# Kernel tuning notes

Hardware: AMD Instinct MI355X
Metric: run time of the kernel (lower is better)

## Reference

```python
import jax, jax.numpy as jnp
import numpy as np

N_BINS = 15
NUM_CLASSES = 16


def _risk_from_H2(u):
    # torch: 0.5*(1 - sqrt(clamp(2*2^-u - 1, min=0)))
    inner = 2.0 * jnp.exp2(-u) - 1.0
    pos = inner > 0.0
    s = jnp.sqrt(jnp.where(pos, inner, 1.0))  # safe sqrt (grad 0 where clamped)
    return 0.5 * (1.0 - jnp.where(pos, s, 0.0))


def setup_inputs() -> dict:
    key = jax.random.key(0)
    k1, k2 = jax.random.split(key)
    N = 4194304
    logits = jax.random.normal(k1, (N, NUM_CLASSES), dtype=jnp.float32)
    labels = jax.random.randint(k2, (N,), 0, NUM_CLASSES)
    return {"logits": logits, "labels": labels}


def reference(logits, labels):
    # logits: [N, C]; labels: [N]
    probs = jax.nn.softmax(logits, axis=-1)                     # [N, C]
    H2 = -jnp.log2((probs * probs).sum(-1) + 1e-12)             # [N]
    err_real = (jnp.argmax(probs, axis=-1) != labels).astype(H2.dtype)  # [N]

    # equal-frequency edges on detached H2 (linear-interp quantiles, as torch.quantile)
    q = jnp.linspace(0.0, 1.0, N_BINS + 1)
    edges = jnp.quantile(jax.lax.stop_gradient(H2), q)
    edges = edges.at[-1].add(1e-6)
    lo, hi = edges[:-1], edges[1:]                              # [n_bins]

    # vectorized replacement of the per-bin Python loop: [n_bins, N] mask
    mask = (H2[None, :] > lo[:, None]) & (H2[None, :] <= hi[:, None])
    maskf = mask.astype(H2.dtype)
    cnt = maskf.sum(-1)                                         # [n_bins]
    safe = jnp.maximum(cnt, 1.0)
    u_bar = (maskf @ H2) / safe                                 # masked means
    err_bar = (maskf @ err_real) / safe
    gaps = jnp.where(cnt > 0.0, jnp.abs(err_bar - _risk_from_H2(u_bar)), 0.0)
    return gaps.mean()
```

## Files before the change

### kernel.cpp

```cpp
#include <hip/hip_runtime.h>

#define L1_BINS 2048
#define L2_BINS 2048
#define KEY_MAX 4194303u
#define NH2_BLOCKS 1280
#define NMG_BLOCKS 256
#define NREF_BLOCKS 2048

struct Ranks { unsigned int r[32]; };
struct Fracs { float f[16]; };

__device__ __forceinline__ unsigned int wave_iscan(unsigned int s, int lane) {
  unsigned int inc = s;
#pragma unroll
  for (int d = 1; d < 64; d <<= 1) {
    unsigned int u = __shfl_up(inc, d);
    if (lane >= d) inc += u;
  }
  return inc;
}

__global__ __launch_bounds__(256) void k_h2(const float4* __restrict__ lg4,
                                            const int* __restrict__ labels,
                                            unsigned int* __restrict__ keys,
                                            unsigned int* __restrict__ hce,
                                            unsigned int* __restrict__ hos,
                                            unsigned int* __restrict__ dones,
                                            int n) {
  __shared__ unsigned int lce[L1_BINS];
  __shared__ unsigned int los[L1_BINS];
  for (int i = threadIdx.x; i < L1_BINS; i += 256) { lce[i] = 0u; los[i] = 0u; }
  if (blockIdx.x == 0 && threadIdx.x < 3) dones[threadIdx.x] = 0u;
  __syncthreads();
  int tid = blockIdx.x * 256 + threadIdx.x;
  int sub = tid & 3;
  int group = tid >> 2;
  int ngroups = (gridDim.x * 256) >> 2;
  for (int row = group; row < n; row += ngroups) {
    float4 v = lg4[(size_t)row * 4 + sub];
    float m = v.x; int a = 0;
    if (v.y > m) { m = v.y; a = 1; }
    if (v.z > m) { m = v.z; a = 2; }
    if (v.w > m) { m = v.w; a = 3; }
    int gidx = sub * 4 + a;
#pragma unroll
    for (int mask = 1; mask <= 2; mask <<= 1) {
      float om = __shfl_xor(m, mask);
      int oi = __shfl_xor(gidx, mask);
      if (om > m || (om == m && oi < gidx)) { m = om; gidx = oi; }
    }
    float e0 = __expf(v.x - m), e1 = __expf(v.y - m);
    float e2 = __expf(v.z - m), e3 = __expf(v.w - m);
    float Z = e0 + e1 + e2 + e3;
    float S2 = e0 * e0 + e1 * e1 + e2 * e2 + e3 * e3;
#pragma unroll
    for (int mask = 1; mask <= 2; mask <<= 1) {
      Z += __shfl_xor(Z, mask);
      S2 += __shfl_xor(S2, mask);
    }
    if (sub == 0) {
      float r = S2 / (Z * Z) + 1e-12f;
      float h2 = -__log2f(r);
      int ki = (int)(h2 * 1048576.0f);
      unsigned int key = (unsigned int)min(max(ki, 0), (int)KEY_MAX);
      unsigned int er = (gidx != labels[row]) ? 1u : 0u;
      keys[row] = key | (er << 31);
      int b = key >> 11;
      atomicAdd(&lce[b], 1u | (er << 16));
      atomicAdd(&los[b], key & 2047u);
    }
  }
  __syncthreads();
  unsigned int* d1 = hce + (size_t)blockIdx.x * L1_BINS;
  unsigned int* d2 = hos + (size_t)blockIdx.x * L1_BINS;
  for (int i = threadIdx.x; i < L1_BINS; i += 256) { d1[i] = lce[i]; d2[i] = los[i]; }
}

__global__ __launch_bounds__(256) void k_merge(const unsigned int* __restrict__ hce,
                                               const unsigned int* __restrict__ hos,
                                               unsigned int* __restrict__ g_cnt,
                                               unsigned int* __restrict__ g_err,
                                               unsigned long long* __restrict__ g_os,
                                               unsigned int* __restrict__ hist2,
                                               unsigned int* __restrict__ dones,
                                               unsigned int* __restrict__ selpfx,
                                               unsigned int* __restrict__ selrank,
                                               Ranks rk) {
  __shared__ unsigned int scnt[32][9], serr[32][9];
  __shared__ unsigned long long sos[32][9];
  __shared__ unsigned int is_last;
  for (int i = threadIdx.x; i < 256; i += 256)
    hist2[blockIdx.x * 256 + i] = 0u;
  int col0 = blockIdx.x * 8;
  int c = threadIdx.x & 7;
  int rg = threadIdx.x >> 3;
  unsigned int acnt = 0, aerr = 0;
  unsigned long long aos = 0ull;
  for (int r = rg; r < NH2_BLOCKS; r += 32) {
    unsigned int v = hce[(size_t)r * L1_BINS + col0 + c];
    acnt += v & 0xFFFFu;
    aerr += v >> 16;
    aos += (unsigned long long)hos[(size_t)r * L1_BINS + col0 + c];
  }
  scnt[rg][c] = acnt; serr[rg][c] = aerr; sos[rg][c] = aos;
  __syncthreads();
  if (threadIdx.x < 8) {
    unsigned int tc = 0, te = 0;
    unsigned long long to = 0ull;
#pragma unroll
    for (int g = 0; g < 32; ++g) { tc += scnt[g][threadIdx.x]; te += serr[g][threadIdx.x]; to += sos[g][threadIdx.x]; }
    g_cnt[col0 + threadIdx.x] = tc;
    g_err[col0 + threadIdx.x] = te;
    g_os[col0 + threadIdx.x] = to;
  }
  __threadfence();
  __syncthreads();
  if (threadIdx.x == 0)
    is_last = (atomicAdd(&dones[0], 1u) == (unsigned int)gridDim.x - 1u) ? 1u : 0u;
  __syncthreads();
  if (!is_last) return;
  __threadfence();
  int wid = threadIdx.x >> 6, lane = threadIdx.x & 63;
  for (int j = wid; j < 32; j += 4) {
    unsigned int rem = rk.r[j];
    unsigned int s = 0;
#pragma unroll 8
    for (int t = 0; t < 32; ++t) s += g_cnt[lane * 32 + t];
    unsigned int inc = wave_iscan(s, lane);
    unsigned int ex = inc - s;
    bool own = (rem >= ex) && (rem < ex + s);
    int src = __ffsll((long long)__ballot(own)) - 1;
    rem -= __shfl(ex, src);
    unsigned int v2 = (lane < 32) ? g_cnt[src * 32 + lane] : 0u;
    unsigned int inc2 = wave_iscan(v2, lane);
    unsigned int ex2 = inc2 - v2;
    bool own2 = (lane < 32) && (rem >= ex2) && (rem < ex2 + v2);
    int s2 = __ffsll((long long)__ballot(own2)) - 1;
    unsigned int ex2s = __shfl(ex2, s2);
    if (lane == 0) {
      selpfx[j] = (unsigned int)(src * 32 + s2);
      selrank[j] = rem - ex2s;
    }
  }
}

__global__ __launch_bounds__(256) void k_refine(const unsigned int* __restrict__ keys,
                                                const unsigned int* __restrict__ selpfx,
                                                unsigned int* __restrict__ hist2,
                                                unsigned int* __restrict__ dones,
                                                const unsigned int* __restrict__ selrank,
                                                const unsigned int* __restrict__ g_cnt,
                                                const unsigned int* __restrict__ g_err,
                                                const unsigned long long* __restrict__ g_os,
                                                float* __restrict__ out,
                                                int n, Fracs fr) {
  __shared__ unsigned char selmap[L1_BINS];
  __shared__ unsigned int sp[32];
  __shared__ unsigned int sv[32];
  __shared__ unsigned int sTT[16];
  __shared__ double SCa[16], SEa[16], SKa[16];
  __shared__ double red[3][4];
  __shared__ unsigned int is_last;
  for (int i = threadIdx.x; i < L1_BINS; i += 256) selmap[i] = 0xFF;
  if (threadIdx.x < 32) sp[threadIdx.x] = selpfx[threadIdx.x];
  __syncthreads();
  if (threadIdx.x == 0) {
    for (int j = 31; j >= 0; --j) selmap[sp[j]] = (unsigned char)j;
  }
  __syncthreads();
  int n4 = n >> 2;
  int stride = gridDim.x * blockDim.x;
  const uint4* k4 = reinterpret_cast<const uint4*>(keys);
  for (int i = blockIdx.x * blockDim.x + threadIdx.x; i < n4; i += stride) {
    uint4 kv = k4[i];
#define REF1(KK) { unsigned int kk = (KK); unsigned int key = kk & KEY_MAX;          \
    unsigned int c = selmap[key >> 11];                                               \
    if (c != 0xFFu) atomicAdd(&hist2[(int)c * L2_BINS + (int)(key & 2047u)],          \
                              1u | ((kk >> 31) << 16)); }
    REF1(kv.x) REF1(kv.y) REF1(kv.z) REF1(kv.w)
#undef REF1
  }
  if (blockIdx.x == 0 && threadIdx.x < (n & 3)) {
    unsigned int kk = keys[(n4 << 2) + threadIdx.x];
    unsigned int key = kk & KEY_MAX;
    unsigned int c = selmap[key >> 11];
    if (c != 0xFFu) atomicAdd(&hist2[(int)c * L2_BINS + (int)(key & 2047u)],
                              1u | ((kk >> 31) << 16));
  }
  __threadfence();
  __syncthreads();
  if (threadIdx.x == 0)
    is_last = (atomicAdd(&dones[1], 1u) == (unsigned int)gridDim.x - 1u) ? 1u : 0u;
  __syncthreads();
  if (!is_last) return;
  __threadfence();
  int wid = threadIdx.x >> 6, lane = threadIdx.x & 63;
  for (int j = wid; j < 32; j += 4) {
    unsigned int rem = selrank[j];
    unsigned int canon = selmap[sp[j]];
    const unsigned int* h = hist2 + (int)canon * L2_BINS;
    unsigned int s = 0;
#pragma unroll 8
    for (int t = 0; t < 32; ++t) s += h[lane * 32 + t] & 0xFFFFu;
    unsigned int inc = wave_iscan(s, lane);
    unsigned int ex = inc - s;
    bool own = (rem >= ex) && (rem < ex + s);
    int src = __ffsll((long long)__ballot(own)) - 1;
    rem -= __shfl(ex, src);
    unsigned int v2 = (lane < 32) ? (h[src * 32 + lane] & 0xFFFFu) : 0u;
    unsigned int inc2 = wave_iscan(v2, lane);
    unsigned int ex2 = inc2 - v2;
    bool own2 = (lane < 32) && (rem >= ex2) && (rem < ex2 + v2);
    int s2 = __ffsll((long long)__ballot(own2)) - 1;
    if (lane == 0) sv[j] = (sp[j] << 11) | (unsigned int)(src * 32 + s2);
  }
  __syncthreads();
  if (threadIdx.x < 16) {
    int i = threadIdx.x;
    float lo = (float)(sv[2 * i] + 1u) * 0x1p-20f;
    float hi = (float)(sv[2 * i + 1] + 1u) * 0x1p-20f;
    float f = fr.f[i];
    float e = lo * (1.0f - f) + hi * f;
    if (i == 15) e += 1e-6f;
    double kdd = (double)e * 1048576.0 - 0.5;
    int T = (int)floor(kdd) + 1;
    while (T > 0 && ((float)(T - 1) + 0.5f) * 0x1p-20f > e) --T;
    while (((float)T + 0.5f) * 0x1p-20f <= e) ++T;
    sTT[i] = (unsigned int)T;
  }
  __syncthreads();
  for (int j = 0; j < 16; ++j) {
    unsigned int T = sTT[j];
    int a1 = (int)(T >> 11);
    int r = (int)(T & 2047u);
    double cd = 0.0, ed = 0.0, kd = 0.0;
    for (int i = threadIdx.x; i < a1; i += 256) {
      double c = (double)g_cnt[i];
      cd += c;
      ed += (double)g_err[i];
      kd += (double)((unsigned long long)i << 11) * c + (double)g_os[i];
    }
    if (a1 < L1_BINS && r > 0) {
      unsigned int canon = selmap[a1];
      if (canon != 0xFFu) {
        const unsigned int* h = hist2 + (int)canon * L2_BINS;
        double base = (double)((unsigned int)a1 << 11);
        for (int s0 = threadIdx.x; s0 < r; s0 += 256) {
          unsigned int ce = h[s0];
          double c = (double)(ce & 0xFFFFu);
          cd += c;
          ed += (double)(ce >> 16);
          kd += c * (base + (double)s0);
        }
      }
    }
    for (int off = 32; off > 0; off >>= 1) {
      cd += __shfl_xor(cd, off);
      ed += __shfl_xor(ed, off);
      kd += __shfl_xor(kd, off);
    }
    if (lane == 0) { red[0][wid] = cd; red[1][wid] = ed; red[2][wid] = kd; }
    __syncthreads();
    if (threadIdx.x == 0) {
      SCa[j] = red[0][0] + red[0][1] + red[0][2] + red[0][3];
      SEa[j] = red[1][0] + red[1][1] + red[1][2] + red[1][3];
      SKa[j] = red[2][0] + red[2][1] + red[2][2] + red[2][3];
    }
    __syncthreads();
  }
  if (threadIdx.x == 0) {
    float g = 0.f;
    for (int b = 0; b < 15; ++b) {
      double cd = SCa[b + 1] - SCa[b];
      double ed = SEa[b + 1] - SEa[b];
      double kd = SKa[b + 1] - SKa[b];
      double safe = cd > 1.0 ? cd : 1.0;
      float u = (float)(((kd + 0.5 * cd) * (1.0 / 1048576.0)) / safe);
      float eb = (float)(ed / safe);
      float inner = 2.0f * exp2f(-u) - 1.0f;
      float s = (inner > 0.f) ? sqrtf(inner) : 0.f;
      float risk = 0.5f * (1.0f - s);
      g += (cd > 0.0) ? fabsf(eb - risk) : 0.f;
    }
    out[0] = g * (1.0f / 15.0f);
  }
}

extern "C" void kernel_launch(void* const* d_in, const int* in_sizes, int n_in,
                              void* d_out, int out_size, void* d_ws, size_t ws_size,
                              hipStream_t stream) {
  const float* logits = (const float*)d_in[0];
  const int* labels = (const int*)d_in[1];
  float* out = (float*)d_out;
  int n = in_sizes[1];

  char* ws = (char*)d_ws;
  size_t offKeys = 0;
  size_t offHce = (size_t)n * 4;
  size_t offHos = offHce + (size_t)NH2_BLOCKS * L1_BINS * 4;
  size_t offGcnt = offHos + (size_t)NH2_BLOCKS * L1_BINS * 4;
  size_t offGerr = offGcnt + (size_t)L1_BINS * 4;
  size_t offGos = offGerr + (size_t)L1_BINS * 4;
  size_t offH2 = offGos + (size_t)L1_BINS * 8;
  size_t offDone = offH2 + (size_t)32 * L2_BINS * 4;
  size_t offSelP = offDone + 16;
  size_t offSelR = offSelP + 128;

  unsigned int* keys = (unsigned int*)(ws + offKeys);
  unsigned int* hce = (unsigned int*)(ws + offHce);
  unsigned int* hos = (unsigned int*)(ws + offHos);
  unsigned int* g_cnt = (unsigned int*)(ws + offGcnt);
  unsigned int* g_err = (unsigned int*)(ws + offGerr);
  unsigned long long* g_os = (unsigned long long*)(ws + offGos);
  unsigned int* hist2 = (unsigned int*)(ws + offH2);
  unsigned int* dones = (unsigned int*)(ws + offDone);
  unsigned int* selp = (unsigned int*)(ws + offSelP);
  unsigned int* selr = (unsigned int*)(ws + offSelR);

  Ranks rk;
  Fracs fr;
  float nm1 = (float)(n - 1);
  for (int i = 0; i < 16; ++i) {
    float q = (i == 15) ? 1.0f : (float)i * (1.0f / 15.0f);
    float idxf = q * nm1;
    float flo = floorf(idxf);
    unsigned int klo = (unsigned int)flo;
    unsigned int khi = (unsigned int)ceilf(idxf);
    unsigned int maxi = (unsigned int)(n - 1);
    if (klo > maxi) klo = maxi;
    if (khi > maxi) khi = maxi;
    rk.r[2 * i] = klo;
    rk.r[2 * i + 1] = khi;
    fr.f[i] = idxf - flo;
  }

  k_h2<<<NH2_BLOCKS, 256, 0, stream>>>((const float4*)logits, labels, keys, hce, hos, dones, n);
  k_merge<<<NMG_BLOCKS, 256, 0, stream>>>(hce, hos, g_cnt, g_err, g_os, hist2, dones, selp, selr, rk);
  k_refine<<<NREF_BLOCKS, 256, 0, stream>>>(keys, selp, hist2, dones, selr, g_cnt, g_err, g_os, out, n, fr);

  (void)n_in; (void)out_size; (void)ws_size;
}
```

Measured before the change: 321.0 us.

## Replace two-level radix select with full-resolution global key histogram

After: 369.7 us. 1.15x slower.

```diff
diff --git a/kernel.cpp b/kernel.cpp
--- a/kernel.cpp
+++ b/kernel.cpp
@@ -1,11 +1,12 @@
 #include <hip/hip_runtime.h>
 
 #define L1_BINS 2048
-#define L2_BINS 2048
+#define L2_SIZE 2048
 #define KEY_MAX 4194303u
-#define NH2_BLOCKS 1280
-#define NMG_BLOCKS 256
-#define NREF_BLOCKS 2048
+#define NKEYS 4194304
+#define NZ_BLOCKS 2048
+#define NH2_BLOCKS 2048
+#define NSUM_BLOCKS 2048
 
 struct Ranks { unsigned int r[32]; };
 struct Fracs { float f[16]; };
@@ -20,18 +21,43 @@
   return inc;
 }
 
+__device__ __forceinline__ unsigned int sel2048(const unsigned int* __restrict__ h,
+                                                bool mask16, unsigned int rem,
+                                                int lane, unsigned int* remOut) {
+  unsigned int s = 0;
+#pragma unroll 8
+  for (int t = 0; t < 32; ++t) {
+    unsigned int v = h[lane * 32 + t];
+    s += mask16 ? (v & 0xFFFFu) : v;
+  }
+  unsigned int inc = wave_iscan(s, lane);
+  unsigned int ex = inc - s;
+  bool own = (rem >= ex) && (rem < ex + s);
+  int src = __ffsll((long long)__ballot(own)) - 1;
+  rem -= __shfl(ex, src);
+  unsigned int v2 = (lane < 32) ? h[src * 32 + lane] : 0u;
+  if (mask16) v2 &= 0xFFFFu;
+  unsigned int inc2 = wave_iscan(v2, lane);
+  unsigned int ex2 = inc2 - v2;
+  bool own2 = (lane < 32) && (rem >= ex2) && (rem < ex2 + v2);
+  int s2 = __ffsll((long long)__ballot(own2)) - 1;
+  *remOut = rem - __shfl(ex2, s2);
+  return (unsigned int)(src * 32 + s2);
+}
+
+__global__ __launch_bounds__(256) void k_zero(uint4* __restrict__ p,
+                                              unsigned int* __restrict__ dones) {
+  int stride = gridDim.x * blockDim.x;
+  int n4 = NKEYS / 4;
+  for (int i = blockIdx.x * blockDim.x + threadIdx.x; i < n4; i += stride)
+    p[i] = make_uint4(0u, 0u, 0u, 0u);
+  if (blockIdx.x == 0 && threadIdx.x < 4) dones[threadIdx.x] = 0u;
+}
+
 __global__ __launch_bounds__(256) void k_h2(const float4* __restrict__ lg4,
                                             const int* __restrict__ labels,
-                                            unsigned int* __restrict__ keys,
-                                            unsigned int* __restrict__ hce,
-                                            unsigned int* __restrict__ hos,
-                                            unsigned int* __restrict__ dones,
+                                            unsigned int* __restrict__ fullhist,
                                             int n) {
-  __shared__ unsigned int lce[L1_BINS];
-  __shared__ unsigned int los[L1_BINS];
-  for (int i = threadIdx.x; i < L1_BINS; i += 256) { lce[i] = 0u; los[i] = 0u; }
-  if (blockIdx.x == 0 && threadIdx.x < 3) dones[threadIdx.x] = 0u;
-  __syncthreads();
   int tid = blockIdx.x * 256 + threadIdx.x;
   int sub = tid & 3;
   int group = tid >> 2;
@@ -64,155 +90,64 @@
       int ki = (int)(h2 * 1048576.0f);
       unsigned int key = (unsigned int)min(max(ki, 0), (int)KEY_MAX);
       unsigned int er = (gidx != labels[row]) ? 1u : 0u;
-      keys[row] = key | (er << 31);
-      int b = key >> 11;
-      atomicAdd(&lce[b], 1u | (er << 16));
-      atomicAdd(&los[b], key & 2047u);
-    }
-  }
-  __syncthreads();
-  unsigned int* d1 = hce + (size_t)blockIdx.x * L1_BINS;
-  unsigned int* d2 = hos + (size_t)blockIdx.x * L1_BINS;
-  for (int i = threadIdx.x; i < L1_BINS; i += 256) { d1[i] = lce[i]; d2[i] = los[i]; }
-}
-
-__global__ __launch_bounds__(256) void k_merge(const unsigned int* __restrict__ hce,
-                                               const unsigned int* __restrict__ hos,
-                                               unsigned int* __restrict__ g_cnt,
-                                               unsigned int* __restrict__ g_err,
-                                               unsigned long long* __restrict__ g_os,
-                                               unsigned int* __restrict__ hist2,
-                                               unsigned int* __restrict__ dones,
-                                               unsigned int* __restrict__ selpfx,
-                                               unsigned int* __restrict__ selrank,
-                                               Ranks rk) {
-  __shared__ unsigned int scnt[32][9], serr[32][9];
-  __shared__ unsigned long long sos[32][9];
-  __shared__ unsigned int is_last;
-  for (int i = threadIdx.x; i < 256; i += 256)
-    hist2[blockIdx.x * 256 + i] = 0u;
-  int col0 = blockIdx.x * 8;
-  int c = threadIdx.x & 7;
-  int rg = threadIdx.x >> 3;
-  unsigned int acnt = 0, aerr = 0;
-  unsigned long long aos = 0ull;
-  for (int r = rg; r < NH2_BLOCKS; r += 32) {
-    unsigned int v = hce[(size_t)r * L1_BINS + col0 + c];
-    acnt += v & 0xFFFFu;
-    aerr += v >> 16;
-    aos += (unsigned long long)hos[(size_t)r * L1_BINS + col0 + c];
-  }
-  scnt[rg][c] = acnt; serr[rg][c] = aerr; sos[rg][c] = aos;
-  __syncthreads();
-  if (threadIdx.x < 8) {
-    unsigned int tc = 0, te = 0;
-    unsigned long long to = 0ull;
-#pragma unroll
-    for (int g = 0; g < 32; ++g) { tc += scnt[g][threadIdx.x]; te += serr[g][threadIdx.x]; to += sos[g][threadIdx.x]; }
-    g_cnt[col0 + threadIdx.x] = tc;
-    g_err[col0 + threadIdx.x] = te;
-    g_os[col0 + threadIdx.x] = to;
-  }
-  __threadfence();
-  __syncthreads();
-  if (threadIdx.x == 0)
-    is_last = (atomicAdd(&dones[0], 1u) == (unsigned int)gridDim.x - 1u) ? 1u : 0u;
-  __syncthreads();
-  if (!is_last) return;
-  __threadfence();
-  int wid = threadIdx.x >> 6, lane = threadIdx.x & 63;
-  for (int j = wid; j < 32; j += 4) {
-    unsigned int rem = rk.r[j];
-    unsigned int s = 0;
-#pragma unroll 8
-    for (int t = 0; t < 32; ++t) s += g_cnt[lane * 32 + t];
-    unsigned int inc = wave_iscan(s, lane);
-    unsigned int ex = inc - s;
-    bool own = (rem >= ex) && (rem < ex + s);
-    int src = __ffsll((long long)__ballot(own)) - 1;
-    rem -= __shfl(ex, src);
-    unsigned int v2 = (lane < 32) ? g_cnt[src * 32 + lane] : 0u;
-    unsigned int inc2 = wave_iscan(v2, lane);
-    unsigned int ex2 = inc2 - v2;
-    bool own2 = (lane < 32) && (rem >= ex2) && (rem < ex2 + v2);
-    int s2 = __ffsll((long long)__ballot(own2)) - 1;
-    unsigned int ex2s = __shfl(ex2, s2);
-    if (lane == 0) {
-      selpfx[j] = (unsigned int)(src * 32 + s2);
-      selrank[j] = rem - ex2s;
-    }
-  }
-}
-
-__global__ __launch_bounds__(256) void k_refine(const unsigned int* __restrict__ keys,
-                                                const unsigned int* __restrict__ selpfx,
-                                                unsigned int* __restrict__ hist2,
-                                                unsigned int* __restrict__ dones,
-                                                const unsigned int* __restrict__ selrank,
-                                                const unsigned int* __restrict__ g_cnt,
-                                                const unsigned int* __restrict__ g_err,
-                                                const unsigned long long* __restrict__ g_os,
-                                                float* __restrict__ out,
-                                                int n, Fracs fr) {
-  __shared__ unsigned char selmap[L1_BINS];
-  __shared__ unsigned int sp[32];
+      atomicAdd(&fullhist[key], 1u | (er << 16));
+    }
+  }
+}
+
+__global__ __launch_bounds__(256) void k_sum(const unsigned int* __restrict__ fullhist,
+                                             unsigned int* __restrict__ g_cnt,
+                                             unsigned int* __restrict__ g_err,
+                                             unsigned long long* __restrict__ g_kk,
+                                             unsigned int* __restrict__ dones,
+                                             float* __restrict__ out,
+                                             Ranks rk, Fracs fr) {
+  __shared__ unsigned int wc[4], we2[4];
+  __shared__ unsigned long long wk[4];
   __shared__ unsigned int sv[32];
   __shared__ unsigned int sTT[16];
   __shared__ double SCa[16], SEa[16], SKa[16];
   __shared__ double red[3][4];
   __shared__ unsigned int is_last;
-  for (int i = threadIdx.x; i < L1_BINS; i += 256) selmap[i] = 0xFF;
-  if (threadIdx.x < 32) sp[threadIdx.x] = selpfx[threadIdx.x];
-  __syncthreads();
-  if (threadIdx.x == 0) {
-    for (int j = 31; j >= 0; --j) selmap[sp[j]] = (unsigned char)j;
-  }
-  __syncthreads();
-  int n4 = n >> 2;
-  int stride = gridDim.x * blockDim.x;
-  const uint4* k4 = reinterpret_cast<const uint4*>(keys);
-  for (int i = blockIdx.x * blockDim.x + threadIdx.x; i < n4; i += stride) {
-    uint4 kv = k4[i];
-#define REF1(KK) { unsigned int kk = (KK); unsigned int key = kk & KEY_MAX;          \
-    unsigned int c = selmap[key >> 11];                                               \
-    if (c != 0xFFu) atomicAdd(&hist2[(int)c * L2_BINS + (int)(key & 2047u)],          \
-                              1u | ((kk >> 31) << 16)); }
-    REF1(kv.x) REF1(kv.y) REF1(kv.z) REF1(kv.w)
-#undef REF1
-  }
-  if (blockIdx.x == 0 && threadIdx.x < (n & 3)) {
-    unsigned int kk = keys[(n4 << 2) + threadIdx.x];
-    unsigned int key = kk & KEY_MAX;
-    unsigned int c = selmap[key >> 11];
-    if (c != 0xFFu) atomicAdd(&hist2[(int)c * L2_BINS + (int)(key & 2047u)],
-                              1u | ((kk >> 31) << 16));
+  int lane = threadIdx.x & 63;
+  int wid = threadIdx.x >> 6;
+  {
+    const unsigned int* slice = fullhist + (size_t)blockIdx.x * L2_SIZE;
+    unsigned int c = 0, e = 0;
+    unsigned long long kk = 0ull;
+    for (int t = threadIdx.x; t < L2_SIZE; t += 256) {
+      unsigned int w = slice[t];
+      unsigned int cc = w & 0xFFFFu;
+      c += cc;
+      e += w >> 16;
+      kk += (unsigned long long)cc * (unsigned long long)t;
+    }
+    for (int off = 32; off > 0; off >>= 1) {
+      c += __shfl_xor(c, off);
+      e += __shfl_xor(e, off);
+      kk += __shfl_xor(kk, off);
+    }
+    if (lane == 0) { wc[wid] = c; we2[wid] = e; wk[wid] = kk; }
+    __syncthreads();
+    if (threadIdx.x == 0) {
+      g_cnt[blockIdx.x] = wc[0] + wc[1] + wc[2] + wc[3];
+      g_err[blockIdx.x] = we2[0] + we2[1] + we2[2] + we2[3];
+      g_kk[blockIdx.x] = wk[0] + wk[1] + wk[2] + wk[3];
+    }
   }
   __threadfence();
   __syncthreads();
   if (threadIdx.x == 0)
-    is_last = (atomicAdd(&dones[1], 1u) == (unsigned int)gridDim.x - 1u) ? 1u : 0u;
+    is_last = (atomicAdd(&dones[0], 1u) == (unsigned int)gridDim.x - 1u) ? 1u : 0u;
   __syncthreads();
   if (!is_last) return;
   __threadfence();
-  int wid = threadIdx.x >> 6, lane = threadIdx.x & 63;
   for (int j = wid; j < 32; j += 4) {
-    unsigned int rem = selrank[j];
-    unsigned int canon = selmap[sp[j]];
-    const unsigned int* h = hist2 + (int)canon * L2_BINS;
-    unsigned int s = 0;
-#pragma unroll 8
-    for (int t = 0; t < 32; ++t) s += h[lane * 32 + t] & 0xFFFFu;
-    unsigned int inc = wave_iscan(s, lane);
-    unsigned int ex = inc - s;
-    bool own = (rem >= ex) && (rem < ex + s);
-    int src = __ffsll((long long)__ballot(own)) - 1;
-    rem -= __shfl(ex, src);
-    unsigned int v2 = (lane < 32) ? (h[src * 32 + lane] & 0xFFFFu) : 0u;
-    unsigned int inc2 = wave_iscan(v2, lane);
-    unsigned int ex2 = inc2 - v2;
-    bool own2 = (lane < 32) && (rem >= ex2) && (rem < ex2 + v2);
-    int s2 = __ffsll((long long)__ballot(own2)) - 1;
-    if (lane == 0) sv[j] = (sp[j] << 11) | (unsigned int)(src * 32 + s2);
+    unsigned int rem;
+    unsigned int a = sel2048(g_cnt, false, rk.r[j], lane, &rem);
+    unsigned int rem2;
+    unsigned int s = sel2048(fullhist + (size_t)a * L2_SIZE, true, rem, lane, &rem2);
+    if (lane == 0) sv[j] = (a << 11) | s;
   }
   __syncthreads();
   if (threadIdx.x < 16) {
@@ -238,20 +173,17 @@
       double c = (double)g_cnt[i];
       cd += c;
       ed += (double)g_err[i];
-      kd += (double)((unsigned long long)i << 11) * c + (double)g_os[i];
+      kd += (double)((unsigned long long)i << 11) * c + (double)g_kk[i];
     }
     if (a1 < L1_BINS && r > 0) {
-      unsigned int canon = selmap[a1];
-      if (canon != 0xFFu) {
-        const unsigned int* h = hist2 + (int)canon * L2_BINS;
-        double base = (double)((unsigned int)a1 << 11);
-        for (int s0 = threadIdx.x; s0 < r; s0 += 256) {
-          unsigned int ce = h[s0];
-          double c = (double)(ce & 0xFFFFu);
-          cd += c;
-          ed += (double)(ce >> 16);
-          kd += c * (base + (double)s0);
-        }
+      const unsigned int* slice = fullhist + (size_t)a1 * L2_SIZE;
+      double base = (double)((unsigned long long)a1 << 11);
+      for (int s0 = threadIdx.x; s0 < r; s0 += 256) {
+        unsigned int w = slice[s0];
+        double c = (double)(w & 0xFFFFu);
+        cd += c;
+        ed += (double)(w >> 16);
+        kd += c * (base + (double)s0);
       }
     }
     for (int off = 32; off > 0; off >>= 1) {
@@ -295,27 +227,17 @@
   int n = in_sizes[1];
 
   char* ws = (char*)d_ws;
-  size_t offKeys = 0;
-  size_t offHce = (size_t)n * 4;
-  size_t offHos = offHce + (size_t)NH2_BLOCKS * L1_BINS * 4;
-  size_t offGcnt = offHos + (size_t)NH2_BLOCKS * L1_BINS * 4;
+  size_t offHist = 0;
+  size_t offGcnt = (size_t)NKEYS * 4;
   size_t offGerr = offGcnt + (size_t)L1_BINS * 4;
-  size_t offGos = offGerr + (size_t)L1_BINS * 4;
-  size_t offH2 = offGos + (size_t)L1_BINS * 8;
-  size_t offDone = offH2 + (size_t)32 * L2_BINS * 4;
-  size_t offSelP = offDone + 16;
-  size_t offSelR = offSelP + 128;
-
-  unsigned int* keys = (unsigned int*)(ws + offKeys);
-  unsigned int* hce = (unsigned int*)(ws + offHce);
-  unsigned int* hos = (unsigned int*)(ws + offHos);
+  size_t offGkk = offGerr + (size_t)L1_BINS * 4;
+  size_t offDone = offGkk + (size_t)L1_BINS * 8;
+
+  unsigned int* fullhist = (unsigned int*)(ws + offHist);
   unsigned int* g_cnt = (unsigned int*)(ws + offGcnt);
   unsigned int* g_err = (unsigned int*)(ws + offGerr);
-  unsigned long long* g_os = (unsigned long long*)(ws + offGos);
-  unsigned int* hist2 = (unsigned int*)(ws + offH2);
+  unsigned long long* g_kk = (unsigned long long*)(ws + offGkk);
   unsigned int* dones = (unsigned int*)(ws + offDone);
-  unsigned int* selp = (unsigned int*)(ws + offSelP);
-  unsigned int* selr = (unsigned int*)(ws + offSelR);
 
   Ranks rk;
   Fracs fr;
@@ -334,9 +256,9 @@
     fr.f[i] = idxf - flo;
   }
 
-  k_h2<<<NH2_BLOCKS, 256, 0, stream>>>((const float4*)logits, labels, keys, hce, hos, dones, n);
-  k_merge<<<NMG_BLOCKS, 256, 0, stream>>>(hce, hos, g_cnt, g_err, g_os, hist2, dones, selp, selr, rk);
-  k_refine<<<NREF_BLOCKS, 256, 0, stream>>>(keys, selp, hist2, dones, selr, g_cnt, g_err, g_os, out, n, fr);
+  k_zero<<<NZ_BLOCKS, 256, 0, stream>>>((uint4*)fullhist, dones);
+  k_h2<<<NH2_BLOCKS, 256, 0, stream>>>((const float4*)logits, labels, fullhist, n);
+  k_sum<<<NSUM_BLOCKS, 256, 0, stream>>>(fullhist, g_cnt, g_err, g_kk, dones, out, rk, fr);
 
   (void)n_in; (void)out_size; (void)ws_size;
 }
```
